# Kernel tuning notes

Hardware: AMD Instinct MI355X
Metric: run time of the kernel (lower is better)

## Reference

```python
import jax, jax.numpy as jnp
import numpy as np

B, S, D, H = 8, 1024, 1024, 16
HD = D // H
EPS = 1e-06


def setup_inputs() -> dict:
    key = jax.random.key(0)
    ks = jax.random.split(key, 10)
    sc = 0.02
    inp = {
        "y": jax.random.normal(ks[0], (B, S, D), dtype=jnp.float32),
        "y_mask": jax.random.randint(ks[1], (B, 1, 1, S), 0, 2) == 1,
        "Wq": jax.random.normal(ks[2], (D, D), dtype=jnp.float32) * sc,
        "bq": jnp.zeros((D,), jnp.float32),
        "Wk": jax.random.normal(ks[3], (D, D), dtype=jnp.float32) * sc,
        "bk": jnp.zeros((D,), jnp.float32),
        "Wv": jax.random.normal(ks[4], (D, D), dtype=jnp.float32) * sc,
        "bv": jnp.zeros((D,), jnp.float32),
        "Wm": jax.random.normal(ks[5], (D, D), dtype=jnp.float32) * sc,
        "bm": jnp.zeros((D,), jnp.float32),
        "a2": jnp.ones((D,), jnp.float32),
        "b2": jnp.zeros((D,), jnp.float32),
    }
    return inp


def _heads(x):
    # [B,S,D] -> [B,H,S,HD]
    return x.reshape(B, S, H, HD).transpose(0, 2, 1, 3)


def reference(y, y_mask, Wq, bq, Wk, bk, Wv, bv, Wm, bm, a2, b2):
    # torch Linear: x @ W^T + b
    q = _heads(y @ Wq.T + bq)
    k = _heads(y @ Wk.T + bk)
    v = _heads(y @ Wv.T + bv)
    scores = jnp.einsum("bhqd,bhkd->bhqk", q, k) / jnp.sqrt(jnp.float32(HD))
    scores = jnp.where(y_mask, jnp.float32(-1e9), scores)
    att = jax.nn.softmax(scores, axis=-1)  # dropout = identity in eval
    atted = jnp.einsum("bhqk,bhkd->bhqd", att, v)
    atted = atted.transpose(0, 2, 1, 3).reshape(B, S, D)
    atted = atted @ Wm.T + bm
    x = y + atted  # residual (dropout1 = identity in eval)
    mean = x.mean(-1, keepdims=True)
    # torch std: unbiased (ddof=1); eps added to std, not variance
    std = jnp.sqrt(((x - mean) ** 2).sum(-1, keepdims=True) / jnp.float32(D - 1))
    return a2 * (x - mean) / (std + EPS) + b2
```

## Files before the change

kernel.cpp:

```cpp
#include <hip/hip_runtime.h>

#define DEVFN __device__ __forceinline__

typedef unsigned short u16;
typedef __attribute__((ext_vector_type(8))) unsigned short u16x8;
typedef __attribute__((ext_vector_type(4))) unsigned short u16x4;
typedef __attribute__((ext_vector_type(8))) __bf16 bf16x8;
typedef __attribute__((ext_vector_type(4))) float f32x4;

DEVFN u16 f2bf(float f) {
    unsigned u = __builtin_bit_cast(unsigned, f);
    u += 0x7FFFu + ((u >> 16) & 1u);
    return (u16)(u >> 16);
}

DEVFN u16 f2bf_hw(float f) {
    return __builtin_bit_cast(u16, (__bf16)f);
}

DEVFN bf16x8 ldfrag(const u16* p) {
    return __builtin_bit_cast(bf16x8, *(const u16x8*)p);
}

DEVFN f32x4 mfma16(bf16x8 a, bf16x8 b, f32x4 c) {
    return __builtin_amdgcn_mfma_f32_16x16x32_bf16(a, b, c, 0, 0, 0);
}

DEVFN void async16(const u16* g, u16* l) {
    __builtin_amdgcn_global_load_lds(
        (const __attribute__((address_space(1))) void*)g,
        (__attribute__((address_space(3))) void*)l, 16, 0, 0);
}

__global__ __launch_bounds__(256) void to_bf16(const float* __restrict__ in,
                                               u16* __restrict__ outp, int n) {
    const int i = (blockIdx.x * 256 + threadIdx.x) * 4;
    if (i >= n) return;
    const float4 v = *(const float4*)&in[i];
    u16x4 o;
    o.x = f2bf(v.x); o.y = f2bf(v.y); o.z = f2bf(v.z); o.w = f2bf(v.w);
    *(u16x4*)&outp[i] = o;
}

__global__ __launch_bounds__(256) void w4_to_bf16(const float* __restrict__ w0,
                                                  const float* __restrict__ w1,
                                                  const float* __restrict__ w2,
                                                  const float* __restrict__ w3,
                                                  u16* __restrict__ outp) {
    const int g = blockIdx.y;
    const float* in = g == 0 ? w0 : (g == 1 ? w1 : (g == 2 ? w2 : w3));
    const int i = (blockIdx.x * 256 + threadIdx.x) * 4;
    const float4 v = *(const float4*)&in[i];
    u16x4 o;
    o.x = f2bf(v.x); o.y = f2bf(v.y); o.z = f2bf(v.z); o.w = f2bf(v.w);
    *(u16x4*)&outp[(size_t)g * 1024 * 1024 + i] = o;
}

template <bool BF16OUT>
__global__ __launch_bounds__(256) void gemm_bt(const u16* __restrict__ A,
                                               const u16* __restrict__ Bt,
                                               const float* __restrict__ b0,
                                               const float* __restrict__ b1,
                                               const float* __restrict__ b2,
                                               void* __restrict__ C0,
                                               void* __restrict__ C1,
                                               void* __restrict__ C2,
                                               int K) {
    __shared__ u16 lA[128 * 32];
    __shared__ u16 lB[128 * 32];
    const int tid = threadIdx.x;
    const int wave = tid >> 6, lane = tid & 63;
    const int quad = lane >> 4, l16 = lane & 15;
    const int m0 = blockIdx.y * 128, n0 = blockIdx.x * 128;
    const int wm = (wave >> 1) * 64, wn = (wave & 1) * 64;
    const int srow = tid >> 2, scol = (tid & 3) * 8;
    const u16* Ag0 = A + (size_t)(m0 + srow) * K + scol;
    const u16* Ag1 = A + (size_t)(m0 + 64 + srow) * K + scol;
    const u16* Bg0 = Bt + (size_t)(n0 + srow) * K + scol;
    const u16* Bg1 = Bt + (size_t)(n0 + 64 + srow) * K + scol;
    u16* lA0 = &lA[wave * 512];
    u16* lA1 = &lA[2048 + wave * 512];
    u16* lB0 = &lB[wave * 512];
    u16* lB1 = &lB[2048 + wave * 512];
    f32x4 acc[4][4] = {};
    for (int k0 = 0; k0 < K; k0 += 32) {
        __syncthreads();
        async16(Ag0 + k0, lA0);
        async16(Ag1 + k0, lA1);
        async16(Bg0 + k0, lB0);
        async16(Bg1 + k0, lB1);
        __syncthreads();
        bf16x8 af[4], bfr[4];
        #pragma unroll
        for (int i = 0; i < 4; ++i)
            af[i] = ldfrag(&lA[(wm + i * 16 + l16) * 32 + quad * 8]);
        #pragma unroll
        for (int i = 0; i < 4; ++i)
            bfr[i] = ldfrag(&lB[(wn + i * 16 + l16) * 32 + quad * 8]);
        #pragma unroll
        for (int mi = 0; mi < 4; ++mi)
            #pragma unroll
            for (int ni = 0; ni < 4; ++ni)
                acc[mi][ni] = mfma16(af[mi], bfr[ni], acc[mi][ni]);
    }
    #pragma unroll
    for (int mi = 0; mi < 4; ++mi) {
        #pragma unroll
        for (int ni = 0; ni < 4; ++ni) {
            const int col = n0 + wn + ni * 16 + l16;
            const int cs = col >> 10;
            const int c = col & 1023;
            const float* bp = cs == 0 ? b0 : (cs == 1 ? b1 : b2);
            void* cpv = cs == 0 ? C0 : (cs == 1 ? C1 : C2);
            const float bb = bp[c];
            #pragma unroll
            for (int r = 0; r < 4; ++r) {
                const int row = m0 + wm + mi * 16 + quad * 4 + r;
                const float v = acc[mi][ni][r] + bb;
                if constexpr (BF16OUT)
                    ((u16*)cpv)[(size_t)row * 1024 + c] = f2bf(v);
                else
                    ((float*)cpv)[(size_t)row * 1024 + c] = v;
            }
        }
    }
}

__global__ __launch_bounds__(256) void transpose_v(const u16* __restrict__ v,
                                                   u16* __restrict__ vt) {
    const int bh = blockIdx.y, bb = bh >> 4, h = bh & 15;
    const int s0 = blockIdx.x * 64;
    __shared__ u16 t[64 * 72];
    const int r = threadIdx.x >> 3, c8 = (threadIdx.x & 7) * 8;
    #pragma unroll
    for (int rr = 0; rr < 64; rr += 32)
        *(u16x8*)&t[(r + rr) * 72 + c8] =
            *(const u16x8*)&v[(size_t)(bb * 1024 + s0 + r + rr) * 1024 + h * 64 + c8];
    __syncthreads();
    #pragma unroll
    for (int rr = 0; rr < 64; rr += 32) {
        u16x8 o;
        #pragma unroll
        for (int j = 0; j < 8; ++j) o[j] = t[(c8 + j) * 72 + (r + rr)];
        *(u16x8*)&vt[(size_t)(bh * 64 + r + rr) * 1024 + s0 + c8] = o;
    }
}

__global__ __launch_bounds__(256) void attn(const u16* __restrict__ qb,
                                            const u16* __restrict__ kb,
                                            const u16* __restrict__ vtb,
                                            const int* __restrict__ mask,
                                            u16* __restrict__ attb) {
    const int lin = blockIdx.x;
    const int xcd = lin & 7, slot = lin >> 3;
    const int bh = xcd * 16 + (slot >> 3);
    const int q0 = (slot & 7) * 128;
    const int bb = bh >> 4, h = bh & 15;
    const int tid = threadIdx.x, wave = tid >> 6, lane = tid & 63;
    const int quad = lane >> 4, l16 = lane & 15;
    __shared__ u16 lK[64 * 72];
    __shared__ u16 lV[64 * 72];
    __shared__ u16 lP[128 * 72];
    __shared__ float lM[1024];

    const int* mrow = mask + bb * 1024;
    for (int i = tid; i < 1024; i += 256) lM[i] = mrow[i] ? -1e9f : 0.0f;

    bf16x8 aq[2][2];
    #pragma unroll
    for (int rg = 0; rg < 2; ++rg) {
        const int qrow = q0 + wave * 32 + rg * 16 + l16;
        const u16* qp = qb + (size_t)(bb * 1024 + qrow) * 1024 + h * 64 + quad * 8;
        aq[rg][0] = ldfrag(qp);
        aq[rg][1] = ldfrag(qp + 32);
    }

    f32x4 o[2][4] = {};
    float ps_acc[2][4] = {};

    const int srow = tid >> 3, scol = (tid & 7) * 8;
    const u16* kbase = kb + (size_t)(bb * 1024) * 1024 + h * 64 + scol;
    const u16* vbase = vtb + (size_t)(bh * 64 + srow) * 1024 + scol;

    u16x8 nk0 = *(const u16x8*)(kbase + (size_t)srow * 1024);
    u16x8 nk1 = *(const u16x8*)(kbase + (size_t)(srow + 32) * 1024);
    u16x8 nv0 = *(const u16x8*)(vbase);
    u16x8 nv1 = *(const u16x8*)(vbase + (size_t)32 * 1024);

    const float C = 0.18033688011112043f;

    for (int kt = 0; kt < 1024; kt += 64) {
        __syncthreads();
        *(u16x8*)&lK[srow * 72 + scol] = nk0;
        *(u16x8*)&lK[(srow + 32) * 72 + scol] = nk1;
        *(u16x8*)&lV[srow * 72 + scol] = nv0;
        *(u16x8*)&lV[(srow + 32) * 72 + scol] = nv1;
        __syncthreads();
        const int ktn = kt + 64;
        if (ktn < 1024) {
            nk0 = *(const u16x8*)(kbase + (size_t)(ktn + srow) * 1024);
            nk1 = *(const u16x8*)(kbase + (size_t)(ktn + srow + 32) * 1024);
            nv0 = *(const u16x8*)(vbase + ktn);
            nv1 = *(const u16x8*)(vbase + (size_t)32 * 1024 + ktn);
        }

        bf16x8 kf[4][2];
        #pragma unroll
        for (int n = 0; n < 4; ++n) {
            kf[n][0] = ldfrag(&lK[(n * 16 + l16) * 72 + quad * 8]);
            kf[n][1] = ldfrag(&lK[(n * 16 + l16) * 72 + 32 + quad * 8]);
        }
        f32x4 s[2][4];
        #pragma unroll
        for (int rg = 0; rg < 2; ++rg)
            #pragma unroll
            for (int n = 0; n < 4; ++n) {
                f32x4 t = {};
                t = mfma16(aq[rg][0], kf[n][0], t);
                t = mfma16(aq[rg][1], kf[n][1], t);
                s[rg][n] = t;
            }
        float bias[4];
        #pragma unroll
        for (int n = 0; n < 4; ++n) bias[n] = lM[kt + n * 16 + l16];
        #pragma unroll
        for (int rg = 0; rg < 2; ++rg)
            #pragma unroll
            for (int n = 0; n < 4; ++n)
                #pragma unroll
                for (int r = 0; r < 4; ++r) {
                    const float p =
                        __builtin_amdgcn_exp2f(__builtin_fmaf(s[rg][n][r], C, bias[n]));
                    ps_acc[rg][r] += p;
                    lP[(wave * 32 + rg * 16 + quad * 4 + r) * 72 + n * 16 + l16] =
                        f2bf_hw(p);
                }
        __asm__ __volatile__("s_waitcnt lgkmcnt(0)" ::: "memory");
        bf16x8 ap[2][2];
        #pragma unroll
        for (int rg = 0; rg < 2; ++rg) {
            ap[rg][0] = ldfrag(&lP[(wave * 32 + rg * 16 + l16) * 72 + quad * 8]);
            ap[rg][1] = ldfrag(&lP[(wave * 32 + rg * 16 + l16) * 72 + 32 + quad * 8]);
        }
        bf16x8 vf[4][2];
        #pragma unroll
        for (int ni = 0; ni < 4; ++ni) {
            vf[ni][0] = ldfrag(&lV[(ni * 16 + l16) * 72 + quad * 8]);
            vf[ni][1] = ldfrag(&lV[(ni * 16 + l16) * 72 + 32 + quad * 8]);
        }
        #pragma unroll
        for (int rg = 0; rg < 2; ++rg)
            #pragma unroll
            for (int ni = 0; ni < 4; ++ni) {
                o[rg][ni] = mfma16(ap[rg][0], vf[ni][0], o[rg][ni]);
                o[rg][ni] = mfma16(ap[rg][1], vf[ni][1], o[rg][ni]);
            }
    }
    #pragma unroll
    for (int off = 1; off < 16; off <<= 1)
        #pragma unroll
        for (int rg = 0; rg < 2; ++rg)
            #pragma unroll
            for (int r = 0; r < 4; ++r)
                ps_acc[rg][r] += __shfl_xor(ps_acc[rg][r], off);
    float rl[2][4];
    #pragma unroll
    for (int rg = 0; rg < 2; ++rg)
        #pragma unroll
        for (int r = 0; r < 4; ++r) rl[rg][r] = 1.f / ps_acc[rg][r];
    #pragma unroll
    for (int rg = 0; rg < 2; ++rg)
        #pragma unroll
        for (int ni = 0; ni < 4; ++ni)
            #pragma unroll
            for (int r = 0; r < 4; ++r) {
                const int row = q0 + wave * 32 + rg * 16 + quad * 4 + r;
                attb[(size_t)(bb * 1024 + row) * 1024 + h * 64 + ni * 16 + l16] =
                    f2bf_hw(o[rg][ni][r] * rl[rg][r]);
            }
}

__global__ __launch_bounds__(256) void ln_res(const float* __restrict__ y,
                                              const float* __restrict__ xp,
                                              const float* __restrict__ a2,
                                              const float* __restrict__ b2,
                                              float* __restrict__ out) {
    const int row = blockIdx.x, tid = threadIdx.x;
    const size_t base = (size_t)row * 1024;
    const int j = tid * 4;
    const float4 yv = *(const float4*)&y[base + j];
    const float4 xv = *(const float4*)&xp[base + j];
    float x[4] = {yv.x + xv.x, yv.y + xv.y, yv.z + xv.z, yv.w + xv.w};
    float s = 0.f, ss = 0.f;
    #pragma unroll
    for (int i = 0; i < 4; ++i) { s += x[i]; ss += x[i] * x[i]; }
    #pragma unroll
    for (int off = 1; off < 64; off <<= 1) {
        s += __shfl_xor(s, off);
        ss += __shfl_xor(ss, off);
    }
    __shared__ float rs[4], rss[4];
    const int wave = tid >> 6, lane = tid & 63;
    if (lane == 0) { rs[wave] = s; rss[wave] = ss; }
    __syncthreads();
    s = rs[0] + rs[1] + rs[2] + rs[3];
    ss = rss[0] + rss[1] + rss[2] + rss[3];
    const float mean = s * (1.f / 1024.f);
    float var = (ss - s * mean) * (1.f / 1023.f);
    var = fmaxf(var, 0.f);
    const float inv = 1.f / (sqrtf(var) + 1e-6f);
    const float4 av = *(const float4*)&a2[j];
    const float4 bv = *(const float4*)&b2[j];
    float4 ov;
    ov.x = av.x * (x[0] - mean) * inv + bv.x;
    ov.y = av.y * (x[1] - mean) * inv + bv.y;
    ov.z = av.z * (x[2] - mean) * inv + bv.z;
    ov.w = av.w * (x[3] - mean) * inv + bv.w;
    *(float4*)&out[base + j] = ov;
}

extern "C" void kernel_launch(void* const* d_in, const int* in_sizes, int n_in,
                              void* d_out, int out_size, void* d_ws, size_t ws_size,
                              hipStream_t stream) {
    (void)in_sizes; (void)n_in; (void)out_size;
    const float* y   = (const float*)d_in[0];
    const int*   msk = (const int*)d_in[1];
    const float* Wq  = (const float*)d_in[2];
    const float* bq  = (const float*)d_in[3];
    const float* Wk  = (const float*)d_in[4];
    const float* bkb = (const float*)d_in[5];
    const float* Wv  = (const float*)d_in[6];
    const float* bv  = (const float*)d_in[7];
    const float* Wm  = (const float*)d_in[8];
    const float* bm  = (const float*)d_in[9];
    const float* a2  = (const float*)d_in[10];
    const float* b2  = (const float*)d_in[11];
    float* out = (float*)d_out;

    char* ws = (char*)d_ws;
    const size_t MB = 1u << 20;
    if (ws_size < 72 * MB) return;
    u16* yb  = (u16*)(ws);
    u16* wqb = (u16*)(ws + 16 * MB);
    u16* wmb = (u16*)(ws + 22 * MB);
    u16* qb  = (u16*)(ws + 24 * MB);
    u16* kb  = (u16*)(ws + 40 * MB);
    u16* vb  = (u16*)(ws + 56 * MB);
    u16* vtb  = yb;
    u16* attb = vb;
    float* xp = (float*)(ws + 24 * MB);

    const int MT = 8192;
    to_bf16<<<MT * 1024 / 1024, 256, 0, stream>>>(y, yb, MT * 1024);
    w4_to_bf16<<<dim3(1024, 4), 256, 0, stream>>>(Wq, Wk, Wv, Wm, wqb);

    gemm_bt<true><<<dim3(24, 64), 256, 0, stream>>>(
        yb, wqb, bq, bkb, bv, qb, kb, vb, 1024);

    transpose_v<<<dim3(16, 128), 256, 0, stream>>>(vb, vtb);
    attn<<<dim3(1024), 256, 0, stream>>>(qb, kb, vtb, msk, attb);

    gemm_bt<false><<<dim3(8, 64), 256, 0, stream>>>(
        attb, wmb, bm, bm, bm, xp, xp, xp, 1024);
    ln_res<<<MT, 256, 0, stream>>>(y, xp, a2, b2, out);
}
```

Baseline: 298.8 us.

## Merge conversions, remap GEMM blocks per XCD, deepen K step, bf16 out-projection

Folds the y and weight fp32-to-bf16 conversions into a single kernel launch. The GEMM now uses a 1D grid remapped so that each XCD owns a contiguous set of N-tiles, which aims to improve L2 reuse of the weight tiles. It also loads 64 K elements per sync round instead of 32, halving the barrier count, at the cost of double the LDS. The out-projection result is now stored as bf16 rather than fp32, cutting write and read traffic into the layernorm, but this adds rounding error before the residual add.

```diff
diff --git a/kernel.cpp b/kernel.cpp
--- a/kernel.cpp
+++ b/kernel.cpp
@@ -18,6 +18,11 @@
     return __builtin_bit_cast(u16, (__bf16)f);
 }
 
+DEVFN float bf2f(u16 h) {
+    unsigned u = (unsigned)h << 16;
+    return __builtin_bit_cast(float, u);
+}
+
 DEVFN bf16x8 ldfrag(const u16* p) {
     return __builtin_bit_cast(bf16x8, *(const u16x8*)p);
 }
@@ -32,76 +37,82 @@
         (__attribute__((address_space(3))) void*)l, 16, 0, 0);
 }
 
-__global__ __launch_bounds__(256) void to_bf16(const float* __restrict__ in,
-                                               u16* __restrict__ outp, int n) {
-    const int i = (blockIdx.x * 256 + threadIdx.x) * 4;
-    if (i >= n) return;
-    const float4 v = *(const float4*)&in[i];
+__global__ __launch_bounds__(256) void conv_all(const float* __restrict__ y,
+                                                const float* __restrict__ w0,
+                                                const float* __restrict__ w1,
+                                                const float* __restrict__ w2,
+                                                const float* __restrict__ w3,
+                                                u16* __restrict__ yb,
+                                                u16* __restrict__ wb) {
+    const int b = blockIdx.x;
+    const float* src;
+    u16* dst;
+    int idx;
+    if (b < 8192) {
+        src = y; dst = yb;
+        idx = b * 1024 + threadIdx.x * 4;
+    } else {
+        const int g = (b - 8192) >> 10;
+        src = g == 0 ? w0 : (g == 1 ? w1 : (g == 2 ? w2 : w3));
+        dst = wb + (size_t)g * 1024 * 1024;
+        idx = ((b - 8192) & 1023) * 1024 + threadIdx.x * 4;
+    }
+    const float4 v = *(const float4*)&src[idx];
     u16x4 o;
     o.x = f2bf(v.x); o.y = f2bf(v.y); o.z = f2bf(v.z); o.w = f2bf(v.w);
-    *(u16x4*)&outp[i] = o;
-}
-
-__global__ __launch_bounds__(256) void w4_to_bf16(const float* __restrict__ w0,
-                                                  const float* __restrict__ w1,
-                                                  const float* __restrict__ w2,
-                                                  const float* __restrict__ w3,
-                                                  u16* __restrict__ outp) {
-    const int g = blockIdx.y;
-    const float* in = g == 0 ? w0 : (g == 1 ? w1 : (g == 2 ? w2 : w3));
-    const int i = (blockIdx.x * 256 + threadIdx.x) * 4;
-    const float4 v = *(const float4*)&in[i];
-    u16x4 o;
-    o.x = f2bf(v.x); o.y = f2bf(v.y); o.z = f2bf(v.z); o.w = f2bf(v.w);
-    *(u16x4*)&outp[(size_t)g * 1024 * 1024 + i] = o;
-}
-
-template <bool BF16OUT>
+    *(u16x4*)&dst[idx] = o;
+}
+
 __global__ __launch_bounds__(256) void gemm_bt(const u16* __restrict__ A,
                                                const u16* __restrict__ Bt,
                                                const float* __restrict__ b0,
                                                const float* __restrict__ b1,
                                                const float* __restrict__ b2,
-                                               void* __restrict__ C0,
-                                               void* __restrict__ C1,
-                                               void* __restrict__ C2,
-                                               int K) {
-    __shared__ u16 lA[128 * 32];
-    __shared__ u16 lB[128 * 32];
+                                               u16* __restrict__ C0,
+                                               u16* __restrict__ C1,
+                                               u16* __restrict__ C2,
+                                               int K, int nPerXcd) {
+    __shared__ u16 lA[2][128 * 32];
+    __shared__ u16 lB[2][128 * 32];
     const int tid = threadIdx.x;
     const int wave = tid >> 6, lane = tid & 63;
     const int quad = lane >> 4, l16 = lane & 15;
-    const int m0 = blockIdx.y * 128, n0 = blockIdx.x * 128;
+    const int blk = blockIdx.x;
+    const int xcd = blk & 7, j = blk >> 3;
+    const int n0 = (xcd * nPerXcd + (j >> 6)) * 128;
+    const int m0 = (j & 63) * 128;
     const int wm = (wave >> 1) * 64, wn = (wave & 1) * 64;
     const int srow = tid >> 2, scol = (tid & 3) * 8;
-    const u16* Ag0 = A + (size_t)(m0 + srow) * K + scol;
-    const u16* Ag1 = A + (size_t)(m0 + 64 + srow) * K + scol;
-    const u16* Bg0 = Bt + (size_t)(n0 + srow) * K + scol;
-    const u16* Bg1 = Bt + (size_t)(n0 + 64 + srow) * K + scol;
-    u16* lA0 = &lA[wave * 512];
-    u16* lA1 = &lA[2048 + wave * 512];
-    u16* lB0 = &lB[wave * 512];
-    u16* lB1 = &lB[2048 + wave * 512];
+    const u16* Ag = A + (size_t)(m0 + srow) * K + scol;
+    const u16* Bg = Bt + (size_t)(n0 + srow) * K + scol;
     f32x4 acc[4][4] = {};
-    for (int k0 = 0; k0 < K; k0 += 32) {
+    for (int k0 = 0; k0 < K; k0 += 64) {
         __syncthreads();
-        async16(Ag0 + k0, lA0);
-        async16(Ag1 + k0, lA1);
-        async16(Bg0 + k0, lB0);
-        async16(Bg1 + k0, lB1);
+        #pragma unroll
+        for (int h = 0; h < 2; ++h)
+            #pragma unroll
+            for (int c = 0; c < 2; ++c) {
+                async16(Ag + k0 + h * 32 + (size_t)(c * 64) * K,
+                        &lA[h][c * 2048 + wave * 512]);
+                async16(Bg + k0 + h * 32 + (size_t)(c * 64) * K,
+                        &lB[h][c * 2048 + wave * 512]);
+            }
         __syncthreads();
-        bf16x8 af[4], bfr[4];
-        #pragma unroll
-        for (int i = 0; i < 4; ++i)
-            af[i] = ldfrag(&lA[(wm + i * 16 + l16) * 32 + quad * 8]);
-        #pragma unroll
-        for (int i = 0; i < 4; ++i)
-            bfr[i] = ldfrag(&lB[(wn + i * 16 + l16) * 32 + quad * 8]);
-        #pragma unroll
-        for (int mi = 0; mi < 4; ++mi)
-            #pragma unroll
-            for (int ni = 0; ni < 4; ++ni)
-                acc[mi][ni] = mfma16(af[mi], bfr[ni], acc[mi][ni]);
+        #pragma unroll
+        for (int kh = 0; kh < 2; ++kh) {
+            bf16x8 af[4], bfr[4];
+            #pragma unroll
+            for (int i = 0; i < 4; ++i)
+                af[i] = ldfrag(&lA[kh][(wm + i * 16 + l16) * 32 + quad * 8]);
+            #pragma unroll
+            for (int i = 0; i < 4; ++i)
+                bfr[i] = ldfrag(&lB[kh][(wn + i * 16 + l16) * 32 + quad * 8]);
+            #pragma unroll
+            for (int mi = 0; mi < 4; ++mi)
+                #pragma unroll
+                for (int ni = 0; ni < 4; ++ni)
+                    acc[mi][ni] = mfma16(af[mi], bfr[ni], acc[mi][ni]);
+        }
     }
     #pragma unroll
     for (int mi = 0; mi < 4; ++mi) {
@@ -111,16 +122,12 @@
             const int cs = col >> 10;
             const int c = col & 1023;
             const float* bp = cs == 0 ? b0 : (cs == 1 ? b1 : b2);
-            void* cpv = cs == 0 ? C0 : (cs == 1 ? C1 : C2);
+            u16* cp = cs == 0 ? C0 : (cs == 1 ? C1 : C2);
             const float bb = bp[c];
             #pragma unroll
             for (int r = 0; r < 4; ++r) {
                 const int row = m0 + wm + mi * 16 + quad * 4 + r;
-                const float v = acc[mi][ni][r] + bb;
-                if constexpr (BF16OUT)
-                    ((u16*)cpv)[(size_t)row * 1024 + c] = f2bf(v);
-                else
-                    ((float*)cpv)[(size_t)row * 1024 + c] = v;
+                cp[(size_t)row * 1024 + c] = f2bf(acc[mi][ni][r] + bb);
             }
         }
     }
@@ -281,7 +288,7 @@
 }
 
 __global__ __launch_bounds__(256) void ln_res(const float* __restrict__ y,
-                                              const float* __restrict__ xp,
+                                              const u16* __restrict__ xpb,
                                               const float* __restrict__ a2,
                                               const float* __restrict__ b2,
                                               float* __restrict__ out) {
@@ -289,8 +296,9 @@
     const size_t base = (size_t)row * 1024;
     const int j = tid * 4;
     const float4 yv = *(const float4*)&y[base + j];
-    const float4 xv = *(const float4*)&xp[base + j];
-    float x[4] = {yv.x + xv.x, yv.y + xv.y, yv.z + xv.z, yv.w + xv.w};
+    const u16x4 xv = *(const u16x4*)&xpb[base + j];
+    float x[4] = {yv.x + bf2f(xv.x), yv.y + bf2f(xv.y),
+                  yv.z + bf2f(xv.z), yv.w + bf2f(xv.w)};
     float s = 0.f, ss = 0.f;
     #pragma unroll
     for (int i = 0; i < 4; ++i) { s += x[i]; ss += x[i] * x[i]; }
@@ -348,19 +356,17 @@
     u16* vb  = (u16*)(ws + 56 * MB);
     u16* vtb  = yb;
     u16* attb = vb;
-    float* xp = (float*)(ws + 24 * MB);
-
-    const int MT = 8192;
-    to_bf16<<<MT * 1024 / 1024, 256, 0, stream>>>(y, yb, MT * 1024);
-    w4_to_bf16<<<dim3(1024, 4), 256, 0, stream>>>(Wq, Wk, Wv, Wm, wqb);
-
-    gemm_bt<true><<<dim3(24, 64), 256, 0, stream>>>(
-        yb, wqb, bq, bkb, bv, qb, kb, vb, 1024);
+    u16* xpb  = qb;
+
+    conv_all<<<12288, 256, 0, stream>>>(y, Wq, Wk, Wv, Wm, yb, wqb);
+
+    gemm_bt<<<1536, 256, 0, stream>>>(
+        yb, wqb, bq, bkb, bv, qb, kb, vb, 1024, 3);
 
     transpose_v<<<dim3(16, 128), 256, 0, stream>>>(vb, vtb);
     attn<<<dim3(1024), 256, 0, stream>>>(qb, kb, vtb, msk, attb);
 
-    gemm_bt<false><<<dim3(8, 64), 256, 0, stream>>>(
-        attb, wmb, bm, bm, bm, xp, xp, xp, 1024);
-    ln_res<<<MT, 256, 0, stream>>>(y, xp, a2, b2, out);
-}
+    gemm_bt<<<512, 256, 0, stream>>>(
+        attb, wmb, bm, bm, bm, xpb, xpb, xpb, 1024, 1);
+    ln_res<<<8192, 256, 0, stream>>>(y, xpb, a2, b2, out);
+}
```

New measurement: 298.3 us. No clear change (-0.2%).
